# Kernel optimization log

Measured on AMD Instinct MI355X. Metric: run time of the kernel, lower is better.

The kernel has to match this reference:

```python
import jax, jax.numpy as jnp
import numpy as np
from jax import lax

DN = ('NCHW', 'OIHW', 'NCHW')


def _conv(x, w, b):
    # SAME-padded 3x3 conv; bias broadcast over spatial dims
    y = lax.conv_general_dilated(x, w, (1, 1), 'SAME', dimension_numbers=DN)
    return y + b[None, :, None, None]


def setup_inputs() -> dict:
    key = jax.random.key(0)
    ks = jax.random.split(key, 6)
    B, Cin, Ch, H, W, K = 8, 16, 32, 256, 256, 3
    fan = (Cin + Ch) * K * K
    scale = 1.0 / np.sqrt(fan)
    return {
        'x': jax.random.normal(ks[0], (B, Cin, H, W), jnp.float32),
        'prev': jax.random.normal(ks[1], (B, Ch, H, W), jnp.float32),
        'mask': jax.random.randint(ks[2], (B, 1, H, W), 0, 2, jnp.int32),
        'w_reset': jax.random.normal(ks[3], (Ch, Cin + Ch, K, K), jnp.float32) * scale,
        'b_reset': jnp.zeros((Ch,), jnp.float32),
        'w_update': jax.random.normal(ks[4], (Ch, Cin + Ch, K, K), jnp.float32) * scale,
        'b_update': jnp.zeros((Ch,), jnp.float32),
        'w_out': jax.random.normal(ks[5], (Ch, Cin + Ch, K, K), jnp.float32) * scale,
        'b_out': jnp.zeros((Ch,), jnp.float32),
    }


def reference(x, prev, mask, w_reset, b_reset, w_update, b_update, w_out, b_out):
    # Dense emulation of submanifold sparse ConvGRU: features exist only at
    # active sites (mask==1); convs gather zeros from inactive sites (matching
    # SCN's rule-based gather) and outputs/biases are masked to active sites.
    m = mask.astype(x.dtype)  # [B,1,H,W] active-site indicator
    x = x * m
    prev = prev * m
    stacked = jnp.concatenate([x, prev], axis=1)  # [B, Cin+Ch, H, W]
    update = jax.nn.sigmoid(_conv(stacked, w_update, b_update)) * m
    reset = jax.nn.sigmoid(_conv(stacked, w_reset, b_reset)) * m
    stacked_r = jnp.concatenate([x, prev * reset], axis=1)
    out_inputs = jnp.tanh(_conv(stacked_r, w_out, b_out)) * m
    # new_state = prev*(1-update) + out_inputs*update (zero off active set)
    new_state = prev * (1.0 - update) + out_inputs * update
    return new_state
```

## Files before the change

kernel.cpp:

```cpp
#include <hip/hip_runtime.h>
#include <hip/hip_bf16.h>
#include <math.h>

#define HH 256
#define WW 256
#define CIN 16
#define CHID 32
#define CST 48
#define HWPIX (HH * WW)

#define TSX 32
#define TSY 16
#define HX 36
#define HY 20
#define NPX (HX * HY)
#define SP 56
#define NKS 14
#define RNX 34
#define RNY 18
#define RPOS (RNX * RNY)
#define EPS 522

typedef unsigned short u16;
typedef unsigned int u32;
typedef __attribute__((ext_vector_type(8))) short short8;
typedef __attribute__((ext_vector_type(8))) __bf16 bf16x8;
typedef __attribute__((ext_vector_type(4))) float f32x4;
typedef __attribute__((ext_vector_type(2))) float f32x2;
typedef __attribute__((ext_vector_type(4))) unsigned int u32x4;

__device__ __forceinline__ float b2f(u16 h) {
    union { unsigned u; float f; } v; v.u = ((unsigned)h) << 16; return v.f;
}
__device__ __forceinline__ u16 f2b(float f) {
    union { float f; unsigned u; } v; v.f = f;
    unsigned r = v.u + 0x7fffu + ((v.u >> 16) & 1u);
    return (u16)(r >> 16);
}
__device__ __forceinline__ u32 pk2(float a, float bq) {
    u32 r;
    asm("v_cvt_pk_bf16_f32 %0, %1, %2" : "=v"(r) : "v"(a), "v"(bq));
    return r;
}
__device__ __forceinline__ int imin(int a, int b) { return a < b ? a : b; }

__global__ void packb_kernel(const float* __restrict__ wR, const float* __restrict__ wU,
                             const float* __restrict__ wO,
                             const float* __restrict__ bR, const float* __restrict__ bU,
                             const float* __restrict__ bO, u16* __restrict__ pB) {
    int i = blockIdx.x * 256 + threadIdx.x;
    const int TOT = 3 * NKS * 2 * 64 * 8;
    if (i >= TOT) return;
    int conv = i / (NKS * 2 * 64 * 8);
    int r = i - conv * (NKS * 2 * 64 * 8);
    int ks = r / (2 * 64 * 8); r -= ks * (2 * 64 * 8);
    int nf = r / (64 * 8);     r -= nf * (64 * 8);
    int lane = r >> 3, j = r & 7;
    int k = ks * 32 + (lane >> 4) * 8 + j;
    int n = nf * 16 + (lane & 15);
    float scale = (conv == 2) ? 2.885390082f : -1.442695041f;
    float val = 0.f;
    if (k < 432) {
        int tap = k / 48, ci = k - tap * 48;
        const float* w = (conv == 0) ? wR : (conv == 1) ? wU : wO;
        val = w[(n * CST + ci) * 9 + tap] * scale;
    } else if (k == 432) {
        const float* bb = (conv == 0) ? bR : (conv == 1) ? bU : bO;
        val = bb[n] * scale;
    }
    pB[i] = f2b(val);
}

__global__ __launch_bounds__(512, 4) void convgru_mfma(
    const float* __restrict__ x, const float* __restrict__ prev,
    const int* __restrict__ mask, const u16* __restrict__ pB,
    float* __restrict__ out)
{
    __shared__ __align__(16) u16 s1[NPX * SP];
    __shared__ unsigned char smask8[NPX];
    float* sEp = (float*)s1;

    const int flat = (blockIdx.z * gridDim.y + blockIdx.y) * gridDim.x + blockIdx.x;
    const int wid  = ((flat & 7) << 7) | (flat >> 3);
    const int b    = wid >> 7;
    const int y0   = ((wid >> 3) & 15) * TSY;
    const int x0   = (wid & 7) * TSX;

    const int tid = threadIdx.x;
    const int w    = tid >> 6;
    const int lane = tid & 63;
    const int run  = lane >> 4;
    const int lo   = lane & 15;

    #pragma unroll
    for (int rp = 0; rp < 2; rp++) {
        int p = rp * 512 + tid;
        bool act = p < NPX;
        int pc = act ? p : (NPX - 1);
        int yy = (pc * 911) >> 15;
        int xx = pc - yy * HX;
        int gy = y0 + yy - 2, gx = x0 + xx - 2;
        bool in = (unsigned)gy < HH && (unsigned)gx < WW;
        int gyc = in ? gy : 0, gxc = in ? gx : 0;
        int mi = in ? mask[(b * HH + gyc) * WW + gxc] : 0;
        if (act) {
            smask8[pc] = (unsigned char)mi;
            u32* dst = (u32*)&s1[pc * SP];
            if (mi) {
                const float* xb = x    + (size_t)b * CIN  * HWPIX + gyc * WW + gxc;
                const float* pb = prev + (size_t)b * CHID * HWPIX + gyc * WW + gxc;
                #pragma unroll
                for (int g = 0; g < 6; g++) {
                    const float* src = (g < 2) ? (xb + g * 8 * HWPIX)
                                               : (pb + (g * 8 - 16) * HWPIX);
                    u32x4 w4;
                    #pragma unroll
                    for (int h = 0; h < 4; h++) {
                        w4[h] = pk2(src[(2 * h) * HWPIX], src[(2 * h + 1) * HWPIX]);
                    }
                    *(u32x4*)(dst + g * 4) = w4;
                }
            } else {
                u32x4 zz = (u32x4){0u, 0u, 0u, 0u};
                #pragma unroll
                for (int g = 0; g < 6; g++) *(u32x4*)(dst + g * 4) = zz;
            }
            *(u32x4*)(dst + 24) = (u32x4){0x3f80u, 0u, 0u, 0u};
        }
    }
    __syncthreads();

    int koff[NKS];
    #pragma unroll
    for (int ks = 0; ks < NKS; ks++) {
        int klin = ks * 4 + run;
        int tap = imin((klin * 43) >> 8, 8);
        int ci  = imin((klin - tap * 6) * 8, 40);
        int ky = (tap * 11) >> 5, kx = tap - ky * 3;
        int off = (((ky * HX + kx) * SP) + ci) * 2;
        if (klin == 54) off = ((HX + 1) * SP + 48) * 2;
        koff[ks] = off;
    }

    const char* s1c = (const char*)s1;
    const short8* pB8 = (const short8*)pB;
    const f32x4 z4 = {0.f, 0.f, 0.f, 0.f};
    const int baseU = (((2 * w) + 1) * HX + 1 + lo) * SP * 2;
    const int fOffB[4] = {0, 16 * SP * 2, HX * SP * 2, (HX + 16) * SP * 2};

    f32x4 accU[4][2];
    #pragma unroll
    for (int f = 0; f < 4; f++) { accU[f][0] = z4; accU[f][1] = z4; }
    {
        short8 bp[2][2];
        bp[0][0] = pB8[(1 * NKS + 0) * 128 + lane];
        bp[0][1] = pB8[(1 * NKS + 0) * 128 + 64 + lane];
        bp[1][0] = pB8[(1 * NKS + 1) * 128 + lane];
        bp[1][1] = pB8[(1 * NKS + 1) * 128 + 64 + lane];
        #pragma unroll
        for (int ks = 0; ks < NKS; ks++) {
            short8 b0 = bp[ks & 1][0], b1 = bp[ks & 1][1];
            if (ks + 2 < NKS) {
                bp[ks & 1][0] = pB8[(1 * NKS + ks + 2) * 128 + lane];
                bp[ks & 1][1] = pB8[(1 * NKS + ks + 2) * 128 + 64 + lane];
            }
            const char* ap = s1c + baseU + koff[ks];
            __builtin_amdgcn_s_setprio(1);
            #pragma unroll
            for (int f = 0; f < 4; f++) {
                short8 av = *(const short8*)(ap + fOffB[f]);
                bf16x8 a = __builtin_bit_cast(bf16x8, av);
                accU[f][0] = __builtin_amdgcn_mfma_f32_16x16x32_bf16(a, __builtin_bit_cast(bf16x8, b0), accU[f][0], 0, 0, 0);
                accU[f][1] = __builtin_amdgcn_mfma_f32_16x16x32_bf16(a, __builtin_bit_cast(bf16x8, b1), accU[f][1], 0, 0, 0);
            }
            __builtin_amdgcn_s_setprio(0);
        }
    }

    f32x4 accR[5][2];
    #pragma unroll
    for (int f = 0; f < 5; f++) { accR[f][0] = z4; accR[f][1] = z4; }

    int pbase[5];
    #pragma unroll
    for (int f = 0; f < 5; f++) {
        int frag = w + f * 8;
        int idx = imin(frag * 16 + lo, RPOS - 1);
        int ry = (idx * 241) >> 13;
        int rx = idx - ry * RNX;
        pbase[f] = (ry * HX + rx) * SP * 2;
    }
    {
        short8 bp[2][2];
        bp[0][0] = pB8[(0 * NKS + 0) * 128 + lane];
        bp[0][1] = pB8[(0 * NKS + 0) * 128 + 64 + lane];
        bp[1][0] = pB8[(0 * NKS + 1) * 128 + lane];
        bp[1][1] = pB8[(0 * NKS + 1) * 128 + 64 + lane];
        #pragma unroll
        for (int ks = 0; ks < NKS; ks++) {
            short8 b0 = bp[ks & 1][0], b1 = bp[ks & 1][1];
            if (ks + 2 < NKS) {
                bp[ks & 1][0] = pB8[(0 * NKS + ks + 2) * 128 + lane];
                bp[ks & 1][1] = pB8[(0 * NKS + ks + 2) * 128 + 64 + lane];
            }
            __builtin_amdgcn_s_setprio(1);
            #pragma unroll
            for (int f = 0; f < 5; f++) {
                if (f == 4 && w == 7) continue;
                short8 av = *(const short8*)(s1c + pbase[f] + koff[ks]);
                bf16x8 a = __builtin_bit_cast(bf16x8, av);
                accR[f][0] = __builtin_amdgcn_mfma_f32_16x16x32_bf16(a, __builtin_bit_cast(bf16x8, b0), accR[f][0], 0, 0, 0);
                accR[f][1] = __builtin_amdgcn_mfma_f32_16x16x32_bf16(a, __builtin_bit_cast(bf16x8, b1), accR[f][1], 0, 0, 0);
            }
            __builtin_amdgcn_s_setprio(0);
        }
    }

    unsigned pms[4][4];
    #pragma unroll
    for (int f = 0; f < 4; f++) {
        int row = 2 * w + (f >> 1);
        int xh  = (f & 1) * 16;
        #pragma unroll
        for (int reg = 0; reg < 4; reg++) {
            int px = xh + run * 4 + reg;
            int base = ((row + 2) * HX + px + 2) * SP + CIN + lo;
            unsigned a0 = s1[base];
            unsigned a1 = s1[base + 16];
            pms[f][reg] = a0 | (a1 << 16);
        }
    }
    __syncthreads();

    {
        #pragma unroll
        for (int f = 0; f < 5; f++) {
            if (f == 4 && w == 7) continue;
            int frag = w + f * 8;
            #pragma unroll
            for (int reg = 0; reg < 4; reg++) {
                int idx = frag * 16 + run * 4 + reg;
                bool valid = idx < RPOS;
                int idc = imin(idx, RPOS - 1);
                int ry = (idc * 241) >> 13, rx = idc - ry * RNX;
                int base = ((ry + 1) * HX + rx + 1) * SP + CIN + lo;
                float sg0 = __builtin_amdgcn_rcpf(1.f + exp2f(accR[f][0][reg]));
                float sg1 = __builtin_amdgcn_rcpf(1.f + exp2f(accR[f][1][reg]));
                float pm0 = b2f(s1[base]);
                float pm1 = b2f(s1[base + 16]);
                u32 pkres = pk2(pm0 * sg0, pm1 * sg1);
                if (valid) {
                    s1[base]      = (u16)pkres;
                    s1[base + 16] = (u16)(pkres >> 16);
                }
            }
        }
    }
    __syncthreads();

    f32x4 accO[4][2];
    #pragma unroll
    for (int f = 0; f < 4; f++) { accO[f][0] = z4; accO[f][1] = z4; }
    {
        short8 bp[2][2];
        bp[0][0] = pB8[(2 * NKS + 0) * 128 + lane];
        bp[0][1] = pB8[(2 * NKS + 0) * 128 + 64 + lane];
        bp[1][0] = pB8[(2 * NKS + 1) * 128 + lane];
        bp[1][1] = pB8[(2 * NKS + 1) * 128 + 64 + lane];
        #pragma unroll
        for (int ks = 0; ks < NKS; ks++) {
            short8 b0 = bp[ks & 1][0], b1 = bp[ks & 1][1];
            if (ks + 2 < NKS) {
                bp[ks & 1][0] = pB8[(2 * NKS + ks + 2) * 128 + lane];
                bp[ks & 1][1] = pB8[(2 * NKS + ks + 2) * 128 + 64 + lane];
            }
            const char* ap = s1c + baseU + koff[ks];
            __builtin_amdgcn_s_setprio(1);
            #pragma unroll
            for (int f = 0; f < 4; f++) {
                short8 av = *(const short8*)(ap + fOffB[f]);
                bf16x8 a = __builtin_bit_cast(bf16x8, av);
                accO[f][0] = __builtin_amdgcn_mfma_f32_16x16x32_bf16(a, __builtin_bit_cast(bf16x8, b0), accO[f][0], 0, 0, 0);
                accO[f][1] = __builtin_amdgcn_mfma_f32_16x16x32_bf16(a, __builtin_bit_cast(bf16x8, b1), accO[f][1], 0, 0, 0);
            }
            __builtin_amdgcn_s_setprio(0);
        }
    }
    __syncthreads();

    {
        #pragma unroll
        for (int f = 0; f < 4; f++) {
            int row = 2 * w + (f >> 1);
            int xh  = (f & 1) * 16;
            #pragma unroll
            for (int rp = 0; rp < 2; rp++) {
                int px0 = xh + run * 4 + rp * 2;
                #pragma unroll
                for (int nf = 0; nf < 2; nf++) {
                    int c = nf * 16 + lo;
                    f32x2 ov;
                    #pragma unroll
                    for (int q = 0; q < 2; q++) {
                        int reg = rp * 2 + q;
                        float mq = (float)smask8[(row + 2) * HX + (xh + run * 4 + reg) + 2];
                        float su = __builtin_amdgcn_rcpf(1.f + exp2f(accU[f][nf][reg]));
                        float th = fmaf(-2.f, __builtin_amdgcn_rcpf(1.f + exp2f(accO[f][nf][reg])), 1.f);
                        float pm = b2f((u16)((pms[f][reg] >> (nf * 16)) & 0xffffu));
                        ov[q] = fmaf(su, fmaf(mq, th, -pm), pm);
                    }
                    *(f32x2*)&sEp[c * EPS + row * TSX + px0] = ov;
                }
            }
        }
    }

    #pragma unroll
    for (int r = 0; r < 8; r++) {
        int i = r * 64 + lane;
        int c   = i >> 4;
        int rr2 = (i >> 3) & 1;
        int q   = (i & 7) * 4;
        int row = 2 * w + rr2;
        f32x4 v = *(const f32x4*)&sEp[c * EPS + row * TSX + q];
        *(f32x4*)&out[((size_t)(b * CHID + c) * HH + y0 + row) * WW + x0 + q] = v;
    }
}

extern "C" void kernel_launch(void* const* d_in, const int* in_sizes, int n_in,
                              void* d_out, int out_size, void* d_ws, size_t ws_size,
                              hipStream_t stream) {
    const float* x       = (const float*)d_in[0];
    const float* prev    = (const float*)d_in[1];
    const int*   mask    = (const int*)d_in[2];
    const float* w_reset = (const float*)d_in[3];
    const float* b_reset = (const float*)d_in[4];
    const float* w_upd   = (const float*)d_in[5];
    const float* b_upd   = (const float*)d_in[6];
    const float* w_out   = (const float*)d_in[7];
    const float* b_out   = (const float*)d_in[8];
    float* out = (float*)d_out;

    u16* pB = (u16*)d_ws;
    const int TOT = 3 * NKS * 2 * 64 * 8;
    packb_kernel<<<(TOT + 255) / 256, 256, 0, stream>>>(w_reset, w_upd, w_out,
                                                        b_reset, b_upd, b_out, pB);

    dim3 grid(WW / TSX, HH / TSY, 8);
    convgru_mfma<<<grid, 512, 0, stream>>>(x, prev, mask, pB, out);
}
```

Measured before the change: 87.60 us.

## Pack update gate to bf16 early, deepen weight prefetch, branchless masked staging

```diff
diff --git a/kernel.cpp b/kernel.cpp
--- a/kernel.cpp
+++ b/kernel.cpp
@@ -103,27 +103,24 @@
         bool in = (unsigned)gy < HH && (unsigned)gx < WW;
         int gyc = in ? gy : 0, gxc = in ? gx : 0;
         int mi = in ? mask[(b * HH + gyc) * WW + gxc] : 0;
+        float mv = (float)mi;
         if (act) {
             smask8[pc] = (unsigned char)mi;
+            const float* xb = x    + (size_t)b * CIN  * HWPIX + gyc * WW + gxc;
+            const float* pb = prev + (size_t)b * CHID * HWPIX + gyc * WW + gxc;
             u32* dst = (u32*)&s1[pc * SP];
-            if (mi) {
-                const float* xb = x    + (size_t)b * CIN  * HWPIX + gyc * WW + gxc;
-                const float* pb = prev + (size_t)b * CHID * HWPIX + gyc * WW + gxc;
+            #pragma unroll
+            for (int g = 0; g < 6; g++) {
+                const float* src = (g < 2) ? (xb + g * 8 * HWPIX)
+                                           : (pb + (g * 8 - 16) * HWPIX);
+                u32x4 w4;
                 #pragma unroll
-                for (int g = 0; g < 6; g++) {
-                    const float* src = (g < 2) ? (xb + g * 8 * HWPIX)
-                                               : (pb + (g * 8 - 16) * HWPIX);
-                    u32x4 w4;
-                    #pragma unroll
-                    for (int h = 0; h < 4; h++) {
-                        w4[h] = pk2(src[(2 * h) * HWPIX], src[(2 * h + 1) * HWPIX]);
-                    }
-                    *(u32x4*)(dst + g * 4) = w4;
+                for (int h = 0; h < 4; h++) {
+                    float v0 = src[(2 * h)     * HWPIX] * mv;
+                    float v1 = src[(2 * h + 1) * HWPIX] * mv;
+                    w4[h] = pk2(v0, v1);
                 }
-            } else {
-                u32x4 zz = (u32x4){0u, 0u, 0u, 0u};
-                #pragma unroll
-                for (int g = 0; g < 6; g++) *(u32x4*)(dst + g * 4) = zz;
+                *(u32x4*)(dst + g * 4) = w4;
             }
             *(u32x4*)(dst + 24) = (u32x4){0x3f80u, 0u, 0u, 0u};
         }
@@ -152,17 +149,19 @@
     #pragma unroll
     for (int f = 0; f < 4; f++) { accU[f][0] = z4; accU[f][1] = z4; }
     {
-        short8 bp[2][2];
-        bp[0][0] = pB8[(1 * NKS + 0) * 128 + lane];
-        bp[0][1] = pB8[(1 * NKS + 0) * 128 + 64 + lane];
-        bp[1][0] = pB8[(1 * NKS + 1) * 128 + lane];
-        bp[1][1] = pB8[(1 * NKS + 1) * 128 + 64 + lane];
+        short8 bp[3][2];
+        #pragma unroll
+        for (int i = 0; i < 3; i++) {
+            bp[i][0] = pB8[(1 * NKS + i) * 128 + lane];
+            bp[i][1] = pB8[(1 * NKS + i) * 128 + 64 + lane];
+        }
         #pragma unroll
         for (int ks = 0; ks < NKS; ks++) {
-            short8 b0 = bp[ks & 1][0], b1 = bp[ks & 1][1];
-            if (ks + 2 < NKS) {
-                bp[ks & 1][0] = pB8[(1 * NKS + ks + 2) * 128 + lane];
-                bp[ks & 1][1] = pB8[(1 * NKS + ks + 2) * 128 + 64 + lane];
+            int slot = ks % 3;
+            short8 b0 = bp[slot][0], b1 = bp[slot][1];
+            if (ks + 3 < NKS) {
+                bp[slot][0] = pB8[(1 * NKS + ks + 3) * 128 + lane];
+                bp[slot][1] = pB8[(1 * NKS + ks + 3) * 128 + 64 + lane];
             }
             const char* ap = s1c + baseU + koff[ks];
             __builtin_amdgcn_s_setprio(1);
@@ -174,6 +173,23 @@
                 accU[f][1] = __builtin_amdgcn_mfma_f32_16x16x32_bf16(a, __builtin_bit_cast(bf16x8, b1), accU[f][1], 0, 0, 0);
             }
             __builtin_amdgcn_s_setprio(0);
+        }
+    }
+
+    unsigned uus[4][4];
+    {
+        #pragma unroll
+        for (int f = 0; f < 4; f++) {
+            int row = 2 * w + (f >> 1);
+            int xh  = (f & 1) * 16;
+            #pragma unroll
+            for (int reg = 0; reg < 4; reg++) {
+                int px = xh + run * 4 + reg;
+                float mq = (float)smask8[(row + 2) * HX + px + 2];
+                float su0 = mq * __builtin_amdgcn_rcpf(1.f + exp2f(accU[f][0][reg]));
+                float su1 = mq * __builtin_amdgcn_rcpf(1.f + exp2f(accU[f][1][reg]));
+                uus[f][reg] = pk2(su0, su1);
+            }
         }
     }
 
@@ -191,17 +207,19 @@
         pbase[f] = (ry * HX + rx) * SP * 2;
     }
     {
-        short8 bp[2][2];
-        bp[0][0] = pB8[(0 * NKS + 0) * 128 + lane];
-        bp[0][1] = pB8[(0 * NKS + 0) * 128 + 64 + lane];
-        bp[1][0] = pB8[(0 * NKS + 1) * 128 + lane];
-        bp[1][1] = pB8[(0 * NKS + 1) * 128 + 64 + lane];
+        short8 bp[3][2];
+        #pragma unroll
+        for (int i = 0; i < 3; i++) {
+            bp[i][0] = pB8[(0 * NKS + i) * 128 + lane];
+            bp[i][1] = pB8[(0 * NKS + i) * 128 + 64 + lane];
+        }
         #pragma unroll
         for (int ks = 0; ks < NKS; ks++) {
-            short8 b0 = bp[ks & 1][0], b1 = bp[ks & 1][1];
-            if (ks + 2 < NKS) {
-                bp[ks & 1][0] = pB8[(0 * NKS + ks + 2) * 128 + lane];
-                bp[ks & 1][1] = pB8[(0 * NKS + ks + 2) * 128 + 64 + lane];
+            int slot = ks % 3;
+            short8 b0 = bp[slot][0], b1 = bp[slot][1];
+            if (ks + 3 < NKS) {
+                bp[slot][0] = pB8[(0 * NKS + ks + 3) * 128 + lane];
+                bp[slot][1] = pB8[(0 * NKS + ks + 3) * 128 + 64 + lane];
             }
             __builtin_amdgcn_s_setprio(1);
             #pragma unroll
@@ -262,17 +280,19 @@
     #pragma unroll
     for (int f = 0; f < 4; f++) { accO[f][0] = z4; accO[f][1] = z4; }
     {
-        short8 bp[2][2];
-        bp[0][0] = pB8[(2 * NKS + 0) * 128 + lane];
-        bp[0][1] = pB8[(2 * NKS + 0) * 128 + 64 + lane];
-        bp[1][0] = pB8[(2 * NKS + 1) * 128 + lane];
-        bp[1][1] = pB8[(2 * NKS + 1) * 128 + 64 + lane];
+        short8 bp[3][2];
+        #pragma unroll
+        for (int i = 0; i < 3; i++) {
+            bp[i][0] = pB8[(2 * NKS + i) * 128 + lane];
+            bp[i][1] = pB8[(2 * NKS + i) * 128 + 64 + lane];
+        }
         #pragma unroll
         for (int ks = 0; ks < NKS; ks++) {
-            short8 b0 = bp[ks & 1][0], b1 = bp[ks & 1][1];
-            if (ks + 2 < NKS) {
-                bp[ks & 1][0] = pB8[(2 * NKS + ks + 2) * 128 + lane];
-                bp[ks & 1][1] = pB8[(2 * NKS + ks + 2) * 128 + 64 + lane];
+            int slot = ks % 3;
+            short8 b0 = bp[slot][0], b1 = bp[slot][1];
+            if (ks + 3 < NKS) {
+                bp[slot][0] = pB8[(2 * NKS + ks + 3) * 128 + lane];
+                bp[slot][1] = pB8[(2 * NKS + ks + 3) * 128 + 64 + lane];
             }
             const char* ap = s1c + baseU + koff[ks];
             __builtin_amdgcn_s_setprio(1);
@@ -294,20 +314,19 @@
             int row = 2 * w + (f >> 1);
             int xh  = (f & 1) * 16;
             #pragma unroll
-            for (int rp = 0; rp < 2; rp++) {
-                int px0 = xh + run * 4 + rp * 2;
+            for (int rp2 = 0; rp2 < 2; rp2++) {
+                int px0 = xh + run * 4 + rp2 * 2;
                 #pragma unroll
                 for (int nf = 0; nf < 2; nf++) {
                     int c = nf * 16 + lo;
                     f32x2 ov;
                     #pragma unroll
                     for (int q = 0; q < 2; q++) {
-                        int reg = rp * 2 + q;
-                        float mq = (float)smask8[(row + 2) * HX + (xh + run * 4 + reg) + 2];
-                        float su = __builtin_amdgcn_rcpf(1.f + exp2f(accU[f][nf][reg]));
+                        int reg = rp2 * 2 + q;
+                        float su = b2f((u16)((uus[f][reg] >> (nf * 16)) & 0xffffu));
                         float th = fmaf(-2.f, __builtin_amdgcn_rcpf(1.f + exp2f(accO[f][nf][reg])), 1.f);
                         float pm = b2f((u16)((pms[f][reg] >> (nf * 16)) & 0xffffu));
-                        ov[q] = fmaf(su, fmaf(mq, th, -pm), pm);
+                        ov[q] = fmaf(su, th - pm, pm);
                     }
                     *(f32x2*)&sEp[c * EPS + row * TSX + px0] = ov;
                 }
```

New measurement: 86.21 us. Within noise of the previous version (-1.6%).

## Store LDS input halo as channel-block planes instead of pixel-major padded rows

Applied to the files above, without the earlier changes.

```diff
diff --git a/kernel.cpp b/kernel.cpp
--- a/kernel.cpp
+++ b/kernel.cpp
@@ -14,12 +14,12 @@
 #define HX 36
 #define HY 20
 #define NPX (HX * HY)
-#define SP 56
 #define NKS 14
 #define RNX 34
 #define RNY 18
 #define RPOS (RNX * RNY)
 #define EPS 522
+
 
 typedef unsigned short u16;
 typedef unsigned int u32;
@@ -76,7 +76,7 @@
     const int* __restrict__ mask, const u16* __restrict__ pB,
     float* __restrict__ out)
 {
-    __shared__ __align__(16) u16 s1[NPX * SP];
+    __shared__ __align__(16) u16 s1[7 * NPX * 8];
     __shared__ unsigned char smask8[NPX];
     float* sEp = (float*)s1;
 
@@ -91,6 +91,7 @@
     const int lane = tid & 63;
     const int run  = lane >> 4;
     const int lo   = lane & 15;
+    const int loh  = lo >> 3, lol = lo & 7;
 
     #pragma unroll
     for (int rp = 0; rp < 2; rp++) {
@@ -103,29 +104,26 @@
         bool in = (unsigned)gy < HH && (unsigned)gx < WW;
         int gyc = in ? gy : 0, gxc = in ? gx : 0;
         int mi = in ? mask[(b * HH + gyc) * WW + gxc] : 0;
+        float mv = (float)mi;
         if (act) {
             smask8[pc] = (unsigned char)mi;
-            u32* dst = (u32*)&s1[pc * SP];
-            if (mi) {
-                const float* xb = x    + (size_t)b * CIN  * HWPIX + gyc * WW + gxc;
-                const float* pb = prev + (size_t)b * CHID * HWPIX + gyc * WW + gxc;
+            const float* xb = x    + (size_t)b * CIN  * HWPIX + gyc * WW + gxc;
+            const float* pb = prev + (size_t)b * CHID * HWPIX + gyc * WW + gxc;
+            u32* dst = (u32*)&s1[pc * 8];
+            #pragma unroll
+            for (int g = 0; g < 6; g++) {
+                const float* src = (g < 2) ? (xb + g * 8 * HWPIX)
+                                           : (pb + (g * 8 - 16) * HWPIX);
+                u32x4 w4;
                 #pragma unroll
-                for (int g = 0; g < 6; g++) {
-                    const float* src = (g < 2) ? (xb + g * 8 * HWPIX)
-                                               : (pb + (g * 8 - 16) * HWPIX);
-                    u32x4 w4;
-                    #pragma unroll
-                    for (int h = 0; h < 4; h++) {
-                        w4[h] = pk2(src[(2 * h) * HWPIX], src[(2 * h + 1) * HWPIX]);
-                    }
-                    *(u32x4*)(dst + g * 4) = w4;
+                for (int h = 0; h < 4; h++) {
+                    float v0 = src[(2 * h)     * HWPIX] * mv;
+                    float v1 = src[(2 * h + 1) * HWPIX] * mv;
+                    w4[h] = pk2(v0, v1);
                 }
-            } else {
-                u32x4 zz = (u32x4){0u, 0u, 0u, 0u};
-                #pragma unroll
-                for (int g = 0; g < 6; g++) *(u32x4*)(dst + g * 4) = zz;
-            }
-            *(u32x4*)(dst + 24) = (u32x4){0x3f80u, 0u, 0u, 0u};
+                *(u32x4*)(dst + g * (NPX * 4)) = w4;
+            }
+            *(u32x4*)(dst + 6 * (NPX * 4)) = (u32x4){0x3f80u, 0u, 0u, 0u};
         }
     }
     __syncthreads();
@@ -135,18 +133,18 @@
     for (int ks = 0; ks < NKS; ks++) {
         int klin = ks * 4 + run;
         int tap = imin((klin * 43) >> 8, 8);
-        int ci  = imin((klin - tap * 6) * 8, 40);
+        int cib = imin(klin - tap * 6, 5);
         int ky = (tap * 11) >> 5, kx = tap - ky * 3;
-        int off = (((ky * HX + kx) * SP) + ci) * 2;
-        if (klin == 54) off = ((HX + 1) * SP + 48) * 2;
+        int off = ((cib * NPX) + ky * HX + kx) * 16;
+        if (klin == 54) off = (6 * NPX) * 16;
         koff[ks] = off;
     }
 
     const char* s1c = (const char*)s1;
     const short8* pB8 = (const short8*)pB;
     const f32x4 z4 = {0.f, 0.f, 0.f, 0.f};
-    const int baseU = (((2 * w) + 1) * HX + 1 + lo) * SP * 2;
-    const int fOffB[4] = {0, 16 * SP * 2, HX * SP * 2, (HX + 16) * SP * 2};
+    const int baseU = (((2 * w) + 1) * HX + 1 + lo) * 16;
+    const int fOffB[4] = {0, 16 * 16, HX * 16, (HX + 16) * 16};
 
     f32x4 accU[4][2];
     #pragma unroll
@@ -188,7 +186,7 @@
         int idx = imin(frag * 16 + lo, RPOS - 1);
         int ry = (idx * 241) >> 13;
         int rx = idx - ry * RNX;
-        pbase[f] = (ry * HX + rx) * SP * 2;
+        pbase[f] = (ry * HX + rx) * 16;
     }
     {
         short8 bp[2][2];
@@ -224,9 +222,9 @@
         #pragma unroll
         for (int reg = 0; reg < 4; reg++) {
             int px = xh + run * 4 + reg;
-            int base = ((row + 2) * HX + px + 2) * SP + CIN + lo;
-            unsigned a0 = s1[base];
-            unsigned a1 = s1[base + 16];
+            int pix = (row + 2) * HX + px + 2;
+            unsigned a0 = s1[((2 + loh) * NPX + pix) * 8 + lol];
+            unsigned a1 = s1[((4 + loh) * NPX + pix) * 8 + lol];
             pms[f][reg] = a0 | (a1 << 16);
         }
     }
@@ -243,15 +241,17 @@
                 bool valid = idx < RPOS;
                 int idc = imin(idx, RPOS - 1);
                 int ry = (idc * 241) >> 13, rx = idc - ry * RNX;
-                int base = ((ry + 1) * HX + rx + 1) * SP + CIN + lo;
+                int pix = (ry + 1) * HX + rx + 1;
+                int base0 = ((2 + loh) * NPX + pix) * 8 + lol;
+                int base1 = ((4 + loh) * NPX + pix) * 8 + lol;
                 float sg0 = __builtin_amdgcn_rcpf(1.f + exp2f(accR[f][0][reg]));
                 float sg1 = __builtin_amdgcn_rcpf(1.f + exp2f(accR[f][1][reg]));
-                float pm0 = b2f(s1[base]);
-                float pm1 = b2f(s1[base + 16]);
+                float pm0 = b2f(s1[base0]);
+                float pm1 = b2f(s1[base1]);
                 u32 pkres = pk2(pm0 * sg0, pm1 * sg1);
                 if (valid) {
-                    s1[base]      = (u16)pkres;
-                    s1[base + 16] = (u16)(pkres >> 16);
+                    s1[base0] = (u16)pkres;
+                    s1[base1] = (u16)(pkres >> 16);
                 }
             }
         }
@@ -294,20 +294,20 @@
             int row = 2 * w + (f >> 1);
             int xh  = (f & 1) * 16;
             #pragma unroll
-            for (int rp = 0; rp < 2; rp++) {
-                int px0 = xh + run * 4 + rp * 2;
+            for (int rp2 = 0; rp2 < 2; rp2++) {
+                int px0 = xh + run * 4 + rp2 * 2;
                 #pragma unroll
                 for (int nf = 0; nf < 2; nf++) {
                     int c = nf * 16 + lo;
                     f32x2 ov;
                     #pragma unroll
                     for (int q = 0; q < 2; q++) {
-                        int reg = rp * 2 + q;
-                        float mq = (float)smask8[(row + 2) * HX + (xh + run * 4 + reg) + 2];
+                        int reg = rp2 * 2 + q;
+                        float mq = (float)smask8[(row + 2) * HX + px0 + q + 2];
                         float su = __builtin_amdgcn_rcpf(1.f + exp2f(accU[f][nf][reg]));
                         float th = fmaf(-2.f, __builtin_amdgcn_rcpf(1.f + exp2f(accO[f][nf][reg])), 1.f);
                         float pm = b2f((u16)((pms[f][reg] >> (nf * 16)) & 0xffffu));
-                        ov[q] = fmaf(su, fmaf(mq, th, -pm), pm);
+                        ov[q] = mq * fmaf(su, th - pm, pm);
                     }
                     *(f32x2*)&sEp[c * EPS + row * TSX + px0] = ov;
                 }
```

New measurement: 87.53 us. No clear change (-0.1%).
